# Kernel optimization log

Measured on AMD Instinct MI355X. Metric: run time of the kernel, lower is better.

Reference implementation:

```python
import jax, jax.numpy as jnp
import numpy as np

DIM = 1024
HEADS = 16
SEQ_H = 32
SEQ_W = 32
HEAD_DIM = DIM // HEADS          # 64
ROT_DIM = HEAD_DIM // 4          # 16 per axis (lucidrains RotaryEmbedding dim)
FULL_ROT = 2 * ROT_DIM           # 32 channels rotated (axial: H-axis + W-axis)


def axial_freqs():
    # lucidrains 'pixel' mode: freqs = linspace(1, max_freq/2, dim//2) * pi, pos = linspace(-1, 1, steps)
    max_freq = SEQ_H * SEQ_W
    base = jnp.linspace(1.0, max_freq / 2.0, ROT_DIM // 2) * jnp.pi  # (rot//2,)
    th = jnp.linspace(-1.0, 1.0, SEQ_H)[:, None] * base[None, :]     # (H, rot//2)
    tw = jnp.linspace(-1.0, 1.0, SEQ_W)[:, None] * base[None, :]     # (W, rot//2)
    fh = jnp.repeat(th, 2, axis=-1)                                   # (H, rot)
    fw = jnpp_repeat = jnp.repeat(tw, 2, axis=-1)                     # (W, rot)
    fh = jnp.broadcast_to(fh[:, None, :], (SEQ_H, SEQ_W, ROT_DIM))
    fw = jnp.broadcast_to(fw[None, :, :], (SEQ_H, SEQ_W, ROT_DIM))
    return jnp.concatenate([fh, fw], axis=-1)                         # (H, W, FULL_ROT)


def rotate_half(t):
    # '... (d r) -> ... d r' with r=2, then (-x2, x1) interleaved back
    x = t.reshape(t.shape[:-1] + (t.shape[-1] // 2, 2))
    x1, x2 = x[..., 0], x[..., 1]
    return jnp.stack([-x2, x1], axis=-1).reshape(t.shape)


def apply_rope(t, cos, sin):
    # t: (B, heads, H, W, head_dim); only first FULL_ROT channels are rotated
    t_rot, t_pass = t[..., :FULL_ROT], t[..., FULL_ROT:]
    t_rot = t_rot * cos + rotate_half(t_rot) * sin
    return jnp.concatenate([t_rot, t_pass], axis=-1)


def setup_inputs() -> dict:
    key = jax.random.key(0)
    k1, k2, k3 = jax.random.split(key, 3)
    B, N = 8, SEQ_H * SEQ_W
    x = jax.random.normal(k1, (B, N, DIM), dtype=jnp.float32)
    Wqkv = jax.random.normal(k2, (3 * DIM, DIM), dtype=jnp.float32) * 0.02
    Wproj = jax.random.normal(k3, (DIM, DIM), dtype=jnp.float32) * 0.02
    bproj = jnp.zeros((DIM,), dtype=jnp.float32)
    return {"x": x, "Wqkv": Wqkv, "Wproj": Wproj, "bproj": bproj}


def reference(x, Wqkv, Wproj, bproj):
    B, N, C = x.shape
    qkv = jnp.einsum('bnc,fc->bnf', x, Wqkv)          # (B, N, 3C)
    q, k, v = jnp.split(qkv, 3, axis=-1)

    def to_grid(t):  # (B, N, C) -> (B, heads, H, W, hd)
        return t.reshape(B, SEQ_H, SEQ_W, HEADS, HEAD_DIM).transpose(0, 3, 1, 2, 4)

    q, k, v = to_grid(q), to_grid(k), to_grid(v)
    freqs = axial_freqs()
    cos, sin = jnp.cos(freqs), jnp.sin(freqs)         # (H, W, FULL_ROT)
    q = apply_rope(q, cos, sin)
    k = apply_rope(k, cos, sin)

    q = q.reshape(B, HEADS, N, HEAD_DIM)
    k = k.reshape(B, HEADS, N, HEAD_DIM)
    v = v.reshape(B, HEADS, N, HEAD_DIM)

    scale = 1.0 / jnp.sqrt(jnp.float32(HEAD_DIM))
    scores = jnp.einsum('bhqd,bhkd->bhqk', q, k) * scale
    attn = jax.nn.softmax(scores, axis=-1)
    out = jnp.einsum('bhqk,bhkd->bhqd', attn, v)       # (B, heads, N, hd)
    out = out.transpose(0, 2, 1, 3).reshape(B, N, C)
    return jnp.einsum('bnc,oc->bno', out, Wproj) + bproj
```

## Files before the change

kernel.cpp:

```cpp
#include <hip/hip_runtime.h>
#include <math.h>

#define DIM_ 1024
#define HEADS_ 16
#define HD_ 64
#define B_ 8
#define N_ 1024
#define M_TOT 8192

typedef __attribute__((ext_vector_type(4))) float f32x4;
typedef _Float16 v8h __attribute__((ext_vector_type(8)));
typedef __attribute__((ext_vector_type(4))) unsigned int u32x4;

static __device__ __forceinline__ unsigned short f2h(float x) {
  _Float16 h = (_Float16)x;
  return __builtin_bit_cast(unsigned short, h);
}
static __device__ __forceinline__ float fexp2(float x) {
  return __builtin_amdgcn_exp2f(x);
}
static __device__ __forceinline__ unsigned pkh2(float a, float b) {
  auto t = __builtin_amdgcn_cvt_pkrtz(a, b);
  return __builtin_bit_cast(unsigned, t);
}

static __device__ __forceinline__ void gload16(unsigned short* lds_base,
                                               const unsigned short* g) {
  __builtin_amdgcn_global_load_lds(
      (const __attribute__((address_space(1))) unsigned int*)g,
      (__attribute__((address_space(3))) unsigned int*)lds_base, 16, 0, 0);
}

static __device__ __forceinline__ void xcd_mf(int hb, int gx, int& by, int& bx) {
  const int xcd = hb & 7;
  const int t = hb >> 3;
  bx = t % gx;
  by = (t / gx) * 8 + xcd;
}

__global__ __launch_bounds__(256) void split_all_k(
    const float* __restrict__ x, const float* __restrict__ wqkv,
    const float* __restrict__ wproj,
    unsigned short* __restrict__ xh, unsigned short* __restrict__ wqh,
    unsigned short* __restrict__ wph) {
  const int i = blockIdx.x * 256 + threadIdx.x;
  const float4* src;
  unsigned short* dst;
  int j;
  if (i < 2097152)      { j = i;           src = (const float4*)x;     dst = xh;  }
  else if (i < 2883584) { j = i - 2097152; src = (const float4*)wqkv;  dst = wqh; }
  else                  { j = i - 2883584; src = (const float4*)wproj; dst = wph; }
  float4 v = src[j];
  ushort4 h;
  h.x = f2h(v.x); h.y = f2h(v.y); h.z = f2h(v.z); h.w = f2h(v.w);
  ((ushort4*)dst)[j] = h;
}

__global__ void rope_table_k(float* cs, float* sn) {
  int i = threadIdx.x;
  if (i < 256) {
    int pos = i >> 3, j = i & 7;
    double u = -1.0 + (double)pos * (2.0/31.0);
    double ang = u * ((1.0 + 73.0*(double)j) * 3.14159265358979323846);
    cs[i] = (float)cos(ang);
    sn[i] = (float)sin(ang);
  }
}

static __device__ __forceinline__ void gemm_core2ph(
    const unsigned short* __restrict__ ah, const unsigned short* __restrict__ bh,
    unsigned short* SM,
    int m0, int f0, f32x4 acc[4][4]) {
  const int tid = threadIdx.x;
  const int w = tid >> 6, l = tid & 63;
  const int lg = l >> 4, lc = l & 15;
  const int wr = w >> 1, wc = w & 1;
  const int r64 = tid >> 2;
  const int ch  = tid & 3;
  const int wof = w * 512;
  const unsigned short* A = ah + (size_t)m0 * 1024;
  const unsigned short* B = bh + (size_t)f0 * 1024;

  auto stg = [&](const unsigned short* base, int t, unsigned short* dst) {
#pragma unroll
    for (int i = 0; i < 2; ++i) {
      const int row = i*64 + r64;
      const int sc = ch ^ ((row >> 1) & 3);
      gload16(dst + i*2048 + wof, base + (size_t)row*1024 + t*32 + sc*8);
    }
  };

  stg(A, 0, SM);
  stg(B, 0, SM + 4096);
  __syncthreads();
#pragma unroll 2
  for (int t = 0; t < 32; ++t) {
    unsigned short* cur = SM + (t & 1) * 8192;
    unsigned short* nxt = SM + ((t & 1) ^ 1) * 8192;
    if (t < 31) {
      stg(A, t + 1, nxt);
      stg(B, t + 1, nxt + 4096);
    }
    v8h a0[4], b0[4];
#pragma unroll
    for (int mi = 0; mi < 4; ++mi) {
      const int row = wr*64 + mi*16 + lc;
      a0[mi] = *(const v8h*)((const char*)cur + row*64 + ((lg ^ ((row >> 1) & 3)) << 4));
    }
#pragma unroll
    for (int nj = 0; nj < 4; ++nj) {
      const int row = wc*64 + nj*16 + lc;
      b0[nj] = *(const v8h*)((const char*)(cur + 4096) + row*64 + ((lg ^ ((row >> 1) & 3)) << 4));
    }
    __builtin_amdgcn_s_setprio(1);
#pragma unroll
    for (int mi = 0; mi < 4; ++mi)
#pragma unroll
      for (int nj = 0; nj < 4; ++nj)
        acc[mi][nj] = __builtin_amdgcn_mfma_f32_16x16x32_f16(a0[mi], b0[nj], acc[mi][nj], 0, 0, 0);
    __builtin_amdgcn_s_setprio(0);
    __syncthreads();
  }
}

__global__ __launch_bounds__(256) void qk_gemm_mfma(
    const unsigned short* __restrict__ xh,
    const unsigned short* __restrict__ wh,
    const float* __restrict__ cs, const float* __restrict__ sn,
    unsigned short* __restrict__ qh, unsigned short* __restrict__ kh) {
  __shared__ unsigned short SM[16384];
  const int tid = threadIdx.x;
  const int w = tid >> 6, l = tid & 63;
  const int lg = l >> 4, lc = l & 15;
  const int wr = w >> 1, wc = w & 1;
  int by, bx;
  xcd_mf(blockIdx.y * gridDim.x + blockIdx.x, 16, by, bx);
  const int m0 = by * 128;
  const int f0 = bx * 128;
  f32x4 acc[4][4] = {};
  gemm_core2ph(xh, wh, SM, m0, f0, acc);
  const int qsel = f0 >> 10;
  const int head = ((f0 & 1023) >> 6) + wc;
  float* tbl = (float*)SM;
  tbl[tid] = cs[tid];
  tbl[256 + tid] = sn[tid];
  __syncthreads();
  const float scale = (qsel == 0) ? 0.18033688011112042f : 1.0f;
  unsigned short* oh = qsel ? kh : qh;
#pragma unroll
  for (int mi = 0; mi < 4; ++mi)
#pragma unroll
    for (int nj = 0; nj < 4; ++nj) {
      const int d = nj*16 + lc;
#pragma unroll
      for (int r = 0; r < 4; ++r) {
        const int m = m0 + wr*64 + mi*16 + lg*4 + r;
        const int b = m >> 10, n = m & 1023;
        float val = acc[mi][nj][r] * scale;
        float part = __shfl_xor(val, 1);
        if (nj < 2) {
          const int p = d >> 1;
          const int pos = (p < 8) ? (n >> 5) : (n & 31);
          const float c = tbl[pos*8 + (p & 7)];
          const float s = tbl[256 + pos*8 + (p & 7)];
          val = (d & 1) ? (val*c + part*s) : (val*c - part*s);
        }
        oh[((size_t)(b*HEADS_ + head)*N_ + n)*HD_ + d] = f2h(val);
      }
    }
}

__global__ __launch_bounds__(256) void v_gemm_mfma(
    const unsigned short* __restrict__ xh, const unsigned short* __restrict__ wh,
    unsigned short* __restrict__ vth) {
  __shared__ unsigned short SM[18432];
  const int tid = threadIdx.x;
  const int w = tid >> 6, l = tid & 63;
  const int lg = l >> 4, lc = l & 15;
  const int wr = w >> 1, wc = w & 1;
  int by, bx;
  xcd_mf(blockIdx.y * gridDim.x + blockIdx.x, 8, by, bx);
  const int m0 = by * 128;
  const int f0 = bx * 128;
  f32x4 acc[4][4] = {};
  gemm_core2ph(xh, wh + (size_t)2048*1024, SM, m0, f0, acc);
  __syncthreads();
  unsigned short* VT = SM + w * 4608;
#pragma unroll
  for (int mi = 0; mi < 4; ++mi)
#pragma unroll
    for (int nj = 0; nj < 4; ++nj)
#pragma unroll
      for (int r = 0; r < 4; r += 2) {
        const int ml = mi*16 + lg*4 + r;
        const int dl = nj*16 + lc;
        *(unsigned*)((char*)VT + dl*144 + ml*2) = pkh2(acc[mi][nj][r], acc[mi][nj][r+1]);
      }
  __syncthreads();
  const int b = m0 >> 10;
  const int n0 = (m0 & 1023) + wr*64;
  const int head = (f0 >> 6) + wc;
#pragma unroll
  for (int j = 0; j < 8; ++j) {
    const int dl = (l >> 3) + j*8;
    u32x4 val = *(const u32x4*)((const char*)VT + dl*144 + (l & 7)*16);
    *(u32x4*)(vth + ((size_t)((b*HEADS_ + head)*HD_ + dl))*N_ + n0 + (l & 7)*8) = val;
  }
}

__global__ __launch_bounds__(256) void proj_gemm_mfma(
    const unsigned short* __restrict__ ah,
    const unsigned short* __restrict__ wh,
    const float* __restrict__ bias, float* __restrict__ out) {
  __shared__ unsigned short SM[16384];
  const int tid = threadIdx.x;
  const int w = tid >> 6, l = tid & 63;
  const int lg = l >> 4, lc = l & 15;
  const int wr = w >> 1, wc = w & 1;
  int by, bx;
  xcd_mf(blockIdx.y * gridDim.x + blockIdx.x, 8, by, bx);
  const int m0 = by * 128;
  const int o0 = bx * 128;
  f32x4 acc[4][4] = {};
  gemm_core2ph(ah, wh, SM, m0, o0, acc);
#pragma unroll
  for (int nj = 0; nj < 4; ++nj) {
    const int o = o0 + wc*64 + nj*16 + lc;
    const float bv = bias[o];
#pragma unroll
    for (int mi = 0; mi < 4; ++mi)
#pragma unroll
      for (int r = 0; r < 4; ++r) {
        const int m = m0 + wr*64 + mi*16 + lg*4 + r;
        out[(size_t)m*DIM_ + o] = acc[mi][nj][r] + bv;
      }
  }
}

__global__ __launch_bounds__(256, 5) void attn_mfma_k(
    const unsigned short* __restrict__ qh,
    const unsigned short* __restrict__ kh,
    const unsigned short* __restrict__ vth,
    unsigned short* __restrict__ aoh) {
  __shared__ unsigned short KhS[8192];
  __shared__ unsigned short VhS[8192];
  const int tid = threadIdx.x;
  const int w = tid >> 6, l = tid & 63;
  const int lg = l >> 4, lc = l & 15;
  const int bh = blockIdx.x, qt = blockIdx.y;
  const size_t gb = (size_t)bh * (N_*HD_);

  v8h qf[2];
#pragma unroll
  for (int c = 0; c < 2; ++c)
    qf[c] = *(const v8h*)(qh + gb +
        (size_t)(qt*64 + w*16 + lc)*HD_ + c*32 + lg*8);
  f32x4 O[4];
#pragma unroll
  for (int dt = 0; dt < 4; ++dt) O[dt] = (f32x4){0.f, 0.f, 0.f, 0.f};
  float lrow = 0.f;

  const int wof = w * 512;
  const int kpr = tid >> 3;
  const int ksc = (tid & 7) ^ (kpr & 7);
  const int vr  = tid >> 4;
  const int vsc = (tid & 15) ^ (vr & 15);

  for (int t = 0; t < 8; ++t) {
#pragma unroll
    for (int i = 0; i < 4; ++i) {
      const int p = i*32 + kpr;
      const int kap = ((p >> 5) << 5) | (((p >> 2) & 3) << 3)
                    | (((p >> 4) & 1) << 2) | (p & 3);
      gload16(KhS + i*2048 + wof, kh + gb + (size_t)(t*128 + kap)*HD_ + ksc*8);
      const int row = i*16 + vr;
      gload16(VhS + i*2048 + wof, vth + gb + (size_t)row*N_ + t*128 + vsc*8);
    }
    __syncthreads();
#pragma unroll
    for (int h = 0; h < 2; ++h) {
      f32x4 s[4];
      __builtin_amdgcn_s_setprio(1);
#pragma unroll
      for (int k4 = 0; k4 < 4; ++k4) {
        s[k4] = (f32x4){0.f, 0.f, 0.f, 0.f};
        const int row = (h*4 + k4)*16 + lc;
        const int sw = (row & 7) << 4;
#pragma unroll
        for (int c = 0; c < 2; ++c) {
          v8h kf = *(const v8h*)((const char*)KhS + row*128 + ((c*64 + lg*16) ^ sw));
          s[k4] = __builtin_amdgcn_mfma_f32_16x16x32_f16(kf, qf[c], s[k4], 0, 0, 0);
        }
      }
      __builtin_amdgcn_s_setprio(0);
      u32x4 pa[2];
#pragma unroll
      for (int cc = 0; cc < 2; ++cc) {
        const float p0 = fexp2(s[2*cc][0]);
        const float p1 = fexp2(s[2*cc][1]);
        const float p2 = fexp2(s[2*cc][2]);
        const float p3 = fexp2(s[2*cc][3]);
        const float p4 = fexp2(s[2*cc+1][0]);
        const float p5 = fexp2(s[2*cc+1][1]);
        const float p6 = fexp2(s[2*cc+1][2]);
        const float p7 = fexp2(s[2*cc+1][3]);
        lrow += ((p0 + p1) + (p2 + p3)) + ((p4 + p5) + (p6 + p7));
        pa[cc] = (u32x4){pkh2(p0, p1), pkh2(p2, p3), pkh2(p4, p5), pkh2(p6, p7)};
      }
      __builtin_amdgcn_s_setprio(1);
#pragma unroll
      for (int dt = 0; dt < 4; ++dt) {
        const int row = dt*16 + lc;
        const int sw = (row & 15) << 4;
#pragma unroll
        for (int cc = 0; cc < 2; ++cc) {
          const int c = h*2 + cc;
          v8h vf = *(const v8h*)((const char*)VhS + row*256 + ((c*64 + lg*16) ^ sw));
          O[dt] = __builtin_amdgcn_mfma_f32_16x16x32_f16(
              __builtin_bit_cast(v8h, pa[cc]), vf, O[dt], 0, 0, 0);
        }
      }
      __builtin_amdgcn_s_setprio(0);
    }
    __syncthreads();
  }
  lrow += __shfl_xor(lrow, 16);
  lrow += __shfl_xor(lrow, 32);
  const int b = bh >> 4, h = bh & 15;
  const float myinv = 1.0f / lrow;
#pragma unroll
  for (int r = 0; r < 4; ++r) {
    const float iv = __shfl(myinv, lg*4 + r);
    const int n = qt*64 + w*16 + lg*4 + r;
    const size_t base = ((size_t)(b*N_ + n))*DIM_ + h*HD_ + lc;
#pragma unroll
    for (int dt = 0; dt < 4; ++dt)
      aoh[base + dt*16] = f2h(O[dt][r] * iv);
  }
}

extern "C" void kernel_launch(void* const* d_in, const int* in_sizes, int n_in,
                              void* d_out, int out_size, void* d_ws, size_t ws_size,
                              hipStream_t stream) {
  const float* x     = (const float*)d_in[0];
  const float* Wqkv  = (const float*)d_in[1];
  const float* Wproj = (const float*)d_in[2];
  const float* bproj = (const float*)d_in[3];
  float* out = (float*)d_out;

  unsigned short* xh  = (unsigned short*)d_ws;
  unsigned short* wqh = xh  + 8388608;
  unsigned short* wph = wqh + 3145728;
  unsigned short* qh  = wph + 1048576;
  unsigned short* kh  = qh  + 8388608;
  unsigned short* vth = kh  + 8388608;
  float* cs = (float*)(vth + 8388608);
  float* sn = cs + 256;
  unsigned short* aoh = xh;

  hipLaunchKernelGGL(rope_table_k, dim3(1), dim3(256), 0, stream, cs, sn);
  hipLaunchKernelGGL(split_all_k, dim3(12288), dim3(256), 0, stream,
                     x, Wqkv, Wproj, xh, wqh, wph);
  hipLaunchKernelGGL(qk_gemm_mfma, dim3(16, 64), dim3(256), 0, stream,
                     xh, wqh, cs, sn, qh, kh);
  hipLaunchKernelGGL(v_gemm_mfma, dim3(8, 64), dim3(256), 0, stream, xh, wqh, vth);
  hipLaunchKernelGGL(attn_mfma_k, dim3(128, 16), dim3(256), 0, stream,
                     qh, kh, vth, aoh);
  hipLaunchKernelGGL(proj_gemm_mfma, dim3(8, 64), dim3(256), 0, stream,
                     aoh, wph, bproj, out);
}
```

Before: 161.6 us.

## Switch GEMM core to three-stage LDS pipeline with vmcnt-based waits

Replaces the double-buffered GEMM main loop with a triple-buffered one that prefetches two K tiles ahead. Each iteration now waits with s_waitcnt vmcnt(4) instead of a full __syncthreads drain, so the next tile's global-to-LDS loads can stay in flight across the barrier. This is meant to hide global memory latency in the QK, V and projection GEMMs. In exchange, LDS use per block rises to 48 KB, which can reduce occupancy, and correctness depends on the async loads issuing exactly four vm ops per stage.

```diff
diff --git a/kernel.cpp b/kernel.cpp
--- a/kernel.cpp
+++ b/kernel.cpp
@@ -67,7 +67,7 @@
   }
 }
 
-static __device__ __forceinline__ void gemm_core2ph(
+static __device__ __forceinline__ void gemm_core3ph(
     const unsigned short* __restrict__ ah, const unsigned short* __restrict__ bh,
     unsigned short* SM,
     int m0, int f0, f32x4 acc[4][4]) {
@@ -90,27 +90,29 @@
     }
   };
 
-  stg(A, 0, SM);
-  stg(B, 0, SM + 4096);
-  __syncthreads();
-#pragma unroll 2
+  stg(A, 0, SM);          stg(B, 0, SM + 4096);
+  stg(A, 1, SM + 8192);   stg(B, 1, SM + 12288);
+  asm volatile("s_waitcnt vmcnt(4)" ::: "memory");
+  __builtin_amdgcn_s_barrier();
+
+  int cur = 0, wsl = 2;
   for (int t = 0; t < 32; ++t) {
-    unsigned short* cur = SM + (t & 1) * 8192;
-    unsigned short* nxt = SM + ((t & 1) ^ 1) * 8192;
-    if (t < 31) {
-      stg(A, t + 1, nxt);
-      stg(B, t + 1, nxt + 4096);
+    unsigned short* cb = SM + cur * 8192;
+    if (t < 30) {
+      unsigned short* nb = SM + wsl * 8192;
+      stg(A, t + 2, nb);
+      stg(B, t + 2, nb + 4096);
     }
     v8h a0[4], b0[4];
 #pragma unroll
     for (int mi = 0; mi < 4; ++mi) {
       const int row = wr*64 + mi*16 + lc;
-      a0[mi] = *(const v8h*)((const char*)cur + row*64 + ((lg ^ ((row >> 1) & 3)) << 4));
+      a0[mi] = *(const v8h*)((const char*)cb + row*64 + ((lg ^ ((row >> 1) & 3)) << 4));
     }
 #pragma unroll
     for (int nj = 0; nj < 4; ++nj) {
       const int row = wc*64 + nj*16 + lc;
-      b0[nj] = *(const v8h*)((const char*)(cur + 4096) + row*64 + ((lg ^ ((row >> 1) & 3)) << 4));
+      b0[nj] = *(const v8h*)((const char*)(cb + 4096) + row*64 + ((lg ^ ((row >> 1) & 3)) << 4));
     }
     __builtin_amdgcn_s_setprio(1);
 #pragma unroll
@@ -119,7 +121,11 @@
       for (int nj = 0; nj < 4; ++nj)
         acc[mi][nj] = __builtin_amdgcn_mfma_f32_16x16x32_f16(a0[mi], b0[nj], acc[mi][nj], 0, 0, 0);
     __builtin_amdgcn_s_setprio(0);
-    __syncthreads();
+    if (t < 30) asm volatile("s_waitcnt vmcnt(4)" ::: "memory");
+    else        asm volatile("s_waitcnt vmcnt(0)" ::: "memory");
+    __builtin_amdgcn_s_barrier();
+    cur = (cur == 2) ? 0 : cur + 1;
+    wsl = (wsl == 2) ? 0 : wsl + 1;
   }
 }
 
@@ -128,7 +134,7 @@
     const unsigned short* __restrict__ wh,
     const float* __restrict__ cs, const float* __restrict__ sn,
     unsigned short* __restrict__ qh, unsigned short* __restrict__ kh) {
-  __shared__ unsigned short SM[16384];
+  __shared__ unsigned short SM[24576];
   const int tid = threadIdx.x;
   const int w = tid >> 6, l = tid & 63;
   const int lg = l >> 4, lc = l & 15;
@@ -138,7 +144,7 @@
   const int m0 = by * 128;
   const int f0 = bx * 128;
   f32x4 acc[4][4] = {};
-  gemm_core2ph(xh, wh, SM, m0, f0, acc);
+  gemm_core3ph(xh, wh, SM, m0, f0, acc);
   const int qsel = f0 >> 10;
   const int head = ((f0 & 1023) >> 6) + wc;
   float* tbl = (float*)SM;
@@ -173,7 +179,7 @@
 __global__ __launch_bounds__(256) void v_gemm_mfma(
     const unsigned short* __restrict__ xh, const unsigned short* __restrict__ wh,
     unsigned short* __restrict__ vth) {
-  __shared__ unsigned short SM[18432];
+  __shared__ unsigned short SM[24576];
   const int tid = threadIdx.x;
   const int w = tid >> 6, l = tid & 63;
   const int lg = l >> 4, lc = l & 15;
@@ -183,7 +189,7 @@
   const int m0 = by * 128;
   const int f0 = bx * 128;
   f32x4 acc[4][4] = {};
-  gemm_core2ph(xh, wh + (size_t)2048*1024, SM, m0, f0, acc);
+  gemm_core3ph(xh, wh + (size_t)2048*1024, SM, m0, f0, acc);
   __syncthreads();
   unsigned short* VT = SM + w * 4608;
 #pragma unroll
@@ -212,7 +218,7 @@
     const unsigned short* __restrict__ ah,
     const unsigned short* __restrict__ wh,
     const float* __restrict__ bias, float* __restrict__ out) {
-  __shared__ unsigned short SM[16384];
+  __shared__ unsigned short SM[24576];
   const int tid = threadIdx.x;
   const int w = tid >> 6, l = tid & 63;
   const int lg = l >> 4, lc = l & 15;
@@ -222,7 +228,7 @@
   const int m0 = by * 128;
   const int o0 = bx * 128;
   f32x4 acc[4][4] = {};
-  gemm_core2ph(ah, wh, SM, m0, o0, acc);
+  gemm_core3ph(ah, wh, SM, m0, o0, acc);
 #pragma unroll
   for (int nj = 0; nj < 4; ++nj) {
     const int o = o0 + wc*64 + nj*16 + lc;
```

Result: slower. 165.9 us (+2.7%).
